# Kernel tuning notes

Measured on AMD Instinct MI355X. Metric: run time of the kernel, lower is better.

Reference implementation:

```python
import jax, jax.numpy as jnp
import numpy as np

B, N, D = 4, 1024, 1024
H, KV, HD = 16, 4, 64
S, CTX = 128, 2048
MLPD = 4096
NITER, DT = 2, 0.1


def _rms(x, w, eps=1e-6):
    return x * jax.lax.rsqrt(jnp.mean(x * x, axis=-1, keepdims=True) + eps) * w


def _gelu(x):
    return jax.nn.gelu(x, approximate=False)  # torch nn.GELU() is exact erf


def _rope(q, k, cos, sin):
    # q: [B,H,N,HD], cos/sin: [N, HD//2]; interleaved-half RoPE as in source
    q1, q2 = q[..., ::2], q[..., 1::2]
    k1, k2 = k[..., ::2], k[..., 1::2]
    c = cos[None, None]
    s = sin[None, None]
    q_rot = jnp.concatenate([q1 * c - q2 * s, q1 * s + q2 * c], axis=-1)
    k_rot = jnp.concatenate([k1 * c - k2 * s, k1 * s + k2 * c], axis=-1)
    return q_rot, k_rot


def setup_inputs():
    key = jax.random.key(0)
    ks = jax.random.split(key, 24)
    rn = lambda k, shp, s=0.02: jax.random.normal(k, shp, jnp.float32) * s
    inv = 1.0 / (10000.0 ** (jnp.arange(0, HD, 2, dtype=jnp.float32) / HD))  # [HD//2]
    ang = jnp.arange(N, dtype=jnp.float32)[:, None] * inv[None, :]
    return {
        'x': jax.random.normal(ks[0], (B, N, D), jnp.float32),
        'c': jax.random.normal(ks[1], (B, D), jnp.float32),
        'context': jax.random.normal(ks[2], (B, S, CTX), jnp.float32),
        'cos': jnp.cos(ang), 'sin': jnp.sin(ang),
        'wq': rn(ks[3], (D, D)), 'wk': rn(ks[4], (D, KV * HD)),
        'wv': rn(ks[5], (D, KV * HD)), 'wo': rn(ks[6], (D, D)),
        'cwq': rn(ks[7], (D, D)), 'cwk': rn(ks[8], (CTX, D)),
        'cwv': rn(ks[9], (CTX, D)), 'cwo': rn(ks[10], (D, D)),
        'fc1_w': rn(ks[11], (D, MLPD)), 'fc1_b': jnp.zeros((MLPD,), jnp.float32),
        'fc2_w': rn(ks[12], (MLPD, D)), 'fc2_b': jnp.zeros((D,), jnp.float32),
        'ada_w': rn(ks[13], (D, 6 * D)), 'ada_b': jnp.zeros((6 * D,), jnp.float32),
        'n1': jnp.ones((D,), jnp.float32), 'n2': jnp.ones((D,), jnp.float32), 'n3': jnp.ones((D,), jnp.float32),
        'int_w': jnp.full((D,), 0.5, jnp.float32), 'mu': jnp.zeros((D,), jnp.float32),
        'hg1_w': rn(ks[14], (D, D // 4)), 'hg1_b': jnp.zeros((D // 4,), jnp.float32),
        'hg2_w': rn(ks[15], (D // 4, 1)), 'hg2_b': jnp.zeros((1,), jnp.float32),
        'ct1_w': rn(ks[16], (2 * D, D // 2)), 'ct1_b': jnp.zeros((D // 2,), jnp.float32),
        'ct2_w': rn(ks[17], (D // 2, 3 * D)), 'ct2_b': jnp.zeros((3 * D,), jnp.float32),
        'rf1_w': rn(ks[18], (D, 2 * D)), 'rf1_b': jnp.zeros((2 * D,), jnp.float32),
        'rf2_w': rn(ks[19], (2 * D, D)), 'rf2_b': jnp.zeros((D,), jnp.float32),
    }


def _forward(x, c, context, cos, sin, wq, wk, wv, wo, cwq, cwk, cwv, cwo,
             fc1_w, fc1_b, fc2_w, fc2_b, ada_w, ada_b, n1, n2, n3, int_w, mu,
             hg1_w, hg1_b, hg2_w, hg2_b, ct1_w, ct1_b, ct2_w, ct2_b,
             rf1_w, rf1_b, rf2_w, rf2_b):
    scale = HD ** -0.5
    # AdaLN-Zero modulation from timestep conditioning c: [B, 6D]
    mod = jax.nn.silu(c) @ ada_w + ada_b
    sh_msa, sc_msa, g_msa, sh_mlp, sc_mlp, g_mlp = jnp.split(mod, 6, axis=-1)
    # --- GQA self-attention with RoPE ---
    h = _rms(x, n1) * (1.0 + sc_msa[:, None, :]) + sh_msa[:, None, :]
    q = (h @ wq).reshape(B, N, H, HD).transpose(0, 2, 1, 3)
    k = (h @ wk).reshape(B, N, KV, HD).transpose(0, 2, 1, 3)
    v = (h @ wv).reshape(B, N, KV, HD).transpose(0, 2, 1, 3)
    q, k = _rope(q, k, cos, sin)
    k = jnp.repeat(k, H // KV, axis=1)  # repeat_interleave over head dim
    v = jnp.repeat(v, H // KV, axis=1)
    attn = jax.nn.softmax(jnp.einsum('bhnd,bhmd->bhnm', q, k) * scale, axis=-1)
    sa = jnp.einsum('bhnm,bhmd->bhnd', attn, v).transpose(0, 2, 1, 3).reshape(B, N, D) @ wo
    x = x + g_msa[:, None, :] * sa
    # --- cross-attention (text conditioning) ---
    h2 = _rms(x, n2)
    qc = (h2 @ cwq).reshape(B, N, H, HD).transpose(0, 2, 1, 3)
    kc = (context @ cwk).reshape(B, S, H, HD).transpose(0, 2, 1, 3)
    vc = (context @ cwv).reshape(B, S, H, HD).transpose(0, 2, 1, 3)
    ca = jax.nn.softmax(jnp.einsum('bhnd,bhsd->bhns', qc, kc) * scale, axis=-1)
    xa = jnp.einsum('bhns,bhsd->bhnd', ca, vc).transpose(0, 2, 1, 3).reshape(B, N, D) @ cwo
    x = x + xa
    # --- AdaLN-modulated MLP ---
    h3 = _rms(x, n3) * (1.0 + sc_mlp[:, None, :]) + sh_mlp[:, None, :]
    m = _gelu(h3 @ fc1_w + fc1_b) @ fc2_w + fc2_b
    x = x + g_mlp[:, None, :] * m
    # --- IntegratorNeuron: damped-oscillator halting dynamics ---
    vst = jnp.zeros_like(x)
    integ = x
    halt_probs = []
    for _ in range(NITER):
        ctrl = _gelu(jnp.concatenate([integ, vst], axis=-1) @ ct1_w + ct1_b) @ ct2_w + ct2_b
        a_raw, b_raw, g_raw = jnp.split(ctrl, 3, axis=-1)
        alpha = jax.nn.sigmoid(a_raw)
        beta = jax.nn.softplus(b_raw)
        gate = jax.nn.sigmoid(g_raw)
        v_next = alpha * vst - beta * (integ - mu)
        x_next = integ + DT * gate * v_next
        hp = jax.nn.sigmoid(_gelu(x_next @ hg1_w + hg1_b) @ hg2_w + hg2_b)  # [B,N,1]
        refined = _gelu(x_next @ rf1_w + rf1_b) @ rf2_w + rf2_b
        integ = integ + hp * refined * int_w
        vst = v_next
        halt_probs.append(hp)
    return integ, jnp.stack(halt_probs, axis=1)


def reference(x, c, context, cos, sin, wq, wk, wv, wo, cwq, cwk, cwv, cwo,
              fc1_w, fc1_b, fc2_w, fc2_b, ada_w, ada_b, n1, n2, n3, int_w, mu,
              hg1_w, hg1_b, hg2_w, hg2_b, ct1_w, ct1_b, ct2_w, ct2_b,
              rf1_w, rf1_b, rf2_w, rf2_b):
    return _forward(x, c, context, cos, sin, wq, wk, wv, wo, cwq, cwk, cwv, cwo,
                    fc1_w, fc1_b, fc2_w, fc2_b, ada_w, ada_b, n1, n2, n3, int_w, mu,
                    hg1_w, hg1_b, hg2_w, hg2_b, ct1_w, ct1_b, ct2_w, ct2_b,
                    rf1_w, rf1_b, rf2_w, rf2_b)
```

## Files before the change

kernel.cpp:

```cpp
#include <hip/hip_runtime.h>
#include <hip/hip_bf16.h>
#include <math.h>

typedef __hip_bfloat16 bf16;
typedef unsigned short ushort;
typedef __bf16 bf16x8 __attribute__((ext_vector_type(8)));
typedef unsigned short u16x8 __attribute__((ext_vector_type(8)));
typedef float f32x4 __attribute__((ext_vector_type(4)));

#define BB 4
#define NN 1024
#define DD 1024
#define HH 16
#define KVH 4
#define HDIM 64
#define SS 128
#define CTXD 2048
#define MLPDIM 4096

__device__ __forceinline__ float bf2f(bf16 v){ return __bfloat162float(v); }
__device__ __forceinline__ bf16 f2bf(float v){ return __float2bfloat16(v); }
__device__ __forceinline__ ushort fbits(float v){ bf16 h = __float2bfloat16(v); return *(ushort*)&h; }
__device__ __forceinline__ float ubf(ushort u){ unsigned int x = ((unsigned int)u) << 16; float f; *(unsigned int*)&f = x; return f; }
__device__ __forceinline__ float sigmf_(float x){ return 1.f/(1.f+expf(-x)); }
__device__ __forceinline__ float geluf_(float x){ return 0.5f*x*(1.f+erff(x*0.70710678118f)); }

typedef const __attribute__((address_space(1))) void* gas_t;
typedef __attribute__((address_space(3))) void* las_t;
__device__ __forceinline__ void gl2lds16(const void* g, void* l){
  __builtin_amdgcn_global_load_lds((gas_t)g, (las_t)l, 16, 0, 0);
}

__global__ void k_copy4(const float4* __restrict__ in, float4* __restrict__ out, int n4){
  int i = blockIdx.x*256 + threadIdx.x;
  if (i < n4) out[i] = in[i];
}
__global__ void k_f2bfv(const float* __restrict__ in, bf16* __restrict__ out, int n){
  int i = blockIdx.x*256 + threadIdx.x;
  if (i < n) out[i] = f2bf(in[i]);
}
__global__ void k_silu(const float* __restrict__ c, float* __restrict__ out, int n){
  int i = blockIdx.x*256 + threadIdx.x;
  if (i < n){ float v = c[i]; out[i] = v*sigmf_(v); }
}
__global__ void k_zero16(unsigned short* __restrict__ p, int n){
  int i = blockIdx.x*256 + threadIdx.x;
  if (i < n) p[i] = 0;
}

__global__ __launch_bounds__(256) void k_wt(const float* __restrict__ in, bf16* __restrict__ out, int K, int N){
  __shared__ float t[64][65];
  int bn = blockIdx.x*64, bk = blockIdx.y*64;
  int tid = threadIdx.x;
  int c4 = (tid & 15)*4, r = tid >> 4;
  #pragma unroll
  for (int i = 0; i < 4; ++i){
    float4 v = *(const float4*)(in + (size_t)(bk + r + i*16)*N + bn + c4);
    t[c4+0][r+i*16] = v.x; t[c4+1][r+i*16] = v.y; t[c4+2][r+i*16] = v.z; t[c4+3][r+i*16] = v.w;
  }
  __syncthreads();
  int n = tid >> 2, k16 = (tid & 3)*16;
  bf16* orow = out + (size_t)(bn + n)*K + bk + k16;
  #pragma unroll
  for (int j = 0; j < 16; ++j) orow[j] = f2bf(t[n][k16 + j]);
}

__global__ void k_adab(const float* __restrict__ b, float* __restrict__ mod, int n){
  int idx = blockIdx.x*256 + threadIdx.x;
  if (idx < n) mod[idx] = b[idx % 6144];
}
__global__ __launch_bounds__(256) void k_ada2(const float* __restrict__ sc, const float* __restrict__ w,
                       float* __restrict__ mod){
  __shared__ float sl[4][32];
  int tid = threadIdx.x;
  int col4 = blockIdx.x*1024 + tid*4;
  int k0 = blockIdx.y*32;
  if (tid < 128) sl[tid >> 5][tid & 31] = sc[(tid >> 5)*DD + k0 + (tid & 31)];
  __syncthreads();
  f32x4 acc[4] = {};
  for (int kk = 0; kk < 32; ++kk){
    const float4 wv4 = *(const float4*)(w + (size_t)(k0 + kk)*6144 + col4);
    #pragma unroll
    for (int b = 0; b < 4; ++b){
      float s = sl[b][kk];
      acc[b][0] += s*wv4.x; acc[b][1] += s*wv4.y; acc[b][2] += s*wv4.z; acc[b][3] += s*wv4.w;
    }
  }
  #pragma unroll
  for (int b = 0; b < 4; ++b)
    #pragma unroll
    for (int j = 0; j < 4; ++j)
      atomicAdd(&mod[(size_t)b*6144 + col4 + j], acc[b][j]);
}

__global__ __launch_bounds__(256) void k_rms(const float* __restrict__ X, const float* __restrict__ w,
                      const float* __restrict__ mod, int sc_off, int sh_off,
                      bf16* __restrict__ out, int use_mod){
  __shared__ float red[256];
  int row = blockIdx.x;
  int b = row >> 10;
  int tid = threadIdx.x;
  const float* xr = X + (size_t)row*DD;
  float s = 0.f;
  #pragma unroll
  for (int i = 0; i < 4; ++i){ float v = xr[tid + i*256]; s += v*v; }
  red[tid] = s; __syncthreads();
  for (int st = 128; st > 0; st >>= 1){ if (tid < st) red[tid] += red[tid+st]; __syncthreads(); }
  float rstd = rsqrtf(red[0]*(1.f/DD) + 1e-6f);
  bf16* orow = out + (size_t)row*DD;
  const float* mrow = use_mod ? (mod + (size_t)b*6*DD) : nullptr;
  #pragma unroll
  for (int i = 0; i < 4; ++i){
    int d = tid + i*256;
    float v = xr[d]*rstd*w[d];
    if (use_mod) v = v*(1.f + mrow[sc_off + d]) + mrow[sh_off + d];
    orow[d] = f2bf(v);
  }
}

__global__ __launch_bounds__(256,2) void k_mm2(const ushort* __restrict__ A, const ushort* __restrict__ BT,
                      const float* __restrict__ bias, ushort* __restrict__ C,
                      int M, int N, int K, int act){
  __shared__ ushort As[128*64];
  __shared__ ushort Bs[128*64];
  int tid = threadIdx.x, lane = tid & 63, wv = tid >> 6;
  int l15 = lane & 15, quad = lane >> 4;
  int bm = blockIdx.y*128, bn = blockIdx.x*128;
  int wm = (wv & 1)*64, wn = (wv >> 1)*64;
  int lr = lane >> 3, lc = lane & 7;
  int ksw = (lc ^ lr) << 3;
  f32x4 acc[4][4] = {};
  const ushort* Abase = A  + (size_t)(bm + wv*32 + lr)*K + ksw;
  const ushort* Bbase = BT + (size_t)(bn + wv*32 + lr)*K + ksw;
  ushort* AsW = As + wv*2048;
  ushort* BsW = Bs + wv*2048;
  int swr = (l15 & 7) << 3;
  for (int k0 = 0; k0 < K; k0 += 64){
    #pragma unroll
    for (int i = 0; i < 4; ++i){
      gl2lds16(Abase + k0 + (size_t)(i*8)*K, AsW + i*512);
      gl2lds16(Bbase + k0 + (size_t)(i*8)*K, BsW + i*512);
    }
    __syncthreads();
    #pragma unroll
    for (int ks = 0; ks < 2; ++ks){
      bf16x8 af[4], bfr[4];
      #pragma unroll
      for (int mi = 0; mi < 4; ++mi){
        int r = wm + mi*16 + l15;
        af[mi] = __builtin_bit_cast(bf16x8, *(const uint4*)(As + r*64 + ((ks*32 + quad*8) ^ swr)));
      }
      #pragma unroll
      for (int nj = 0; nj < 4; ++nj){
        int r = wn + nj*16 + l15;
        bfr[nj] = __builtin_bit_cast(bf16x8, *(const uint4*)(Bs + r*64 + ((ks*32 + quad*8) ^ swr)));
      }
      #pragma unroll
      for (int mi = 0; mi < 4; ++mi)
        #pragma unroll
        for (int nj = 0; nj < 4; ++nj)
          acc[mi][nj] = __builtin_amdgcn_mfma_f32_16x16x32_bf16(af[mi], bfr[nj], acc[mi][nj], 0, 0, 0);
    }
    __syncthreads();
  }
  #pragma unroll
  for (int nj = 0; nj < 4; ++nj){
    int col = bn + wn + nj*16 + l15;
    float bv = bias ? bias[col] : 0.f;
    #pragma unroll
    for (int mi = 0; mi < 4; ++mi){
      #pragma unroll
      for (int r = 0; r < 4; ++r){
        int row = bm + wm + mi*16 + quad*4 + r;
        float v = acc[mi][nj][r] + bv;
        if (act) v = geluf_(v);
        C[(size_t)row*N + col] = fbits(v);
      }
    }
  }
}

__global__ __launch_bounds__(256,2) void k_mm2h(const ushort* __restrict__ A, const ushort* __restrict__ BT,
                      const float* __restrict__ bias, ushort* __restrict__ C,
                      int M, int N, int K, int act){
  __shared__ ushort As[128*64];
  __shared__ ushort Bs[64*64];
  int tid = threadIdx.x, lane = tid & 63, wv = tid >> 6;
  int l15 = lane & 15, quad = lane >> 4;
  int bm = blockIdx.y*128, bn = blockIdx.x*64;
  int wm = wv*32;
  int lr = lane >> 3, lc = lane & 7;
  int ksw = (lc ^ lr) << 3;
  f32x4 acc[2][4] = {};
  const ushort* Abase = A  + (size_t)(bm + wv*32 + lr)*K + ksw;
  const ushort* Bbase = BT + (size_t)(bn + wv*16 + lr)*K + ksw;
  ushort* AsW = As + wv*2048;
  ushort* BsW = Bs + wv*1024;
  int swr = (l15 & 7) << 3;
  for (int k0 = 0; k0 < K; k0 += 64){
    #pragma unroll
    for (int i = 0; i < 4; ++i)
      gl2lds16(Abase + k0 + (size_t)(i*8)*K, AsW + i*512);
    #pragma unroll
    for (int i = 0; i < 2; ++i)
      gl2lds16(Bbase + k0 + (size_t)(i*8)*K, BsW + i*512);
    __syncthreads();
    #pragma unroll
    for (int ks = 0; ks < 2; ++ks){
      bf16x8 af[2], bfr[4];
      #pragma unroll
      for (int mi = 0; mi < 2; ++mi){
        int r = wm + mi*16 + l15;
        af[mi] = __builtin_bit_cast(bf16x8, *(const uint4*)(As + r*64 + ((ks*32 + quad*8) ^ swr)));
      }
      #pragma unroll
      for (int nj = 0; nj < 4; ++nj){
        int r = nj*16 + l15;
        bfr[nj] = __builtin_bit_cast(bf16x8, *(const uint4*)(Bs + r*64 + ((ks*32 + quad*8) ^ swr)));
      }
      #pragma unroll
      for (int mi = 0; mi < 2; ++mi)
        #pragma unroll
        for (int nj = 0; nj < 4; ++nj)
          acc[mi][nj] = __builtin_amdgcn_mfma_f32_16x16x32_bf16(af[mi], bfr[nj], acc[mi][nj], 0, 0, 0);
    }
    __syncthreads();
  }
  #pragma unroll
  for (int nj = 0; nj < 4; ++nj){
    int col = bn + nj*16 + l15;
    float bv = bias ? bias[col] : 0.f;
    #pragma unroll
    for (int mi = 0; mi < 2; ++mi){
      #pragma unroll
      for (int r = 0; r < 4; ++r){
        int row = bm + wm + mi*16 + quad*4 + r;
        float v = acc[mi][nj][r] + bv;
        if (act) v = geluf_(v);
        C[(size_t)row*N + col] = fbits(v);
      }
    }
  }
}

__global__ void k_rope(const bf16* __restrict__ in, const float* __restrict__ cw,
                       const float* __restrict__ sw, bf16* __restrict__ out, int NHp, int n){
  int idx = blockIdx.x*256 + threadIdx.x;
  if (idx >= n) return;
  int d2 = idx & 31; int t = idx >> 5;
  int nn = t % NN; t /= NN; int h = t % NHp; int b = t / NHp;
  const bf16* base = in + ((size_t)((b*NN+nn)*NHp + h))*HDIM;
  float e = bf2f(base[2*d2]), o = bf2f(base[2*d2+1]);
  float c = cw[nn*32 + d2], s = sw[nn*32 + d2];
  bf16* ob = out + ((size_t)((b*NHp+h)*NN + nn))*HDIM;
  ob[d2]      = f2bf(e*c - o*s);
  ob[32 + d2] = f2bf(e*s + o*c);
}

__global__ void k_tr(const bf16* __restrict__ in, bf16* __restrict__ out, int T, int NHp, int n){
  int idx = blockIdx.x*256 + threadIdx.x;
  if (idx >= n) return;
  int d = idx & 63; int t = idx >> 6;
  int h = t % NHp; t /= NHp; int tok = t % T; int b = t / T;
  out[((size_t)((b*NHp+h)*T + tok))*64 + d] = in[idx];
}

__global__ void k_trv(const bf16* __restrict__ in, bf16* __restrict__ out, int T, int NHp, int n){
  int idx = blockIdx.x*256 + threadIdx.x;
  if (idx >= n) return;
  int d = idx & 63; int t = idx >> 6;
  int h = t % NHp; t /= NHp; int tok = t % T; int b = t / T;
  out[((size_t)(b*NHp+h)*64 + d)*T + tok] = in[idx];
}

__global__ __launch_bounds__(256) void k_fattn(const ushort* __restrict__ Q, const ushort* __restrict__ K,
                      const ushort* __restrict__ V, ushort* __restrict__ O,
                      int NH, int NKV, int Nq, int Nk, float scale){
  __shared__ ushort Kt[64*64];
  __shared__ ushort Vt[64*64];
  __shared__ ushort Ps[4][16*72];
  int tid = threadIdx.x, lane = tid & 63, wv = tid >> 6;
  int l15 = lane & 15, quad = lane >> 4;
  int lr = lane >> 3, lc = lane & 7;
  int ksw = (lc ^ lr) << 3;
  int swr = (l15 & 7) << 3;
  int nqt = Nq >> 6;
  int qt = blockIdx.x % nqt; int t = blockIdx.x / nqt; int h = t % NH; int b = t / NH;
  int kvh = h / (NH / NKV);
  const ushort* Kb = K + (size_t)(b*NKV+kvh)*Nk*64 + ksw;
  const ushort* Vb = V + (size_t)(b*NKV+kvh)*64*Nk + ksw;
  const ushort* Qp = Q + ((size_t)((b*NH+h)*Nq + qt*64 + wv*16 + l15))*64;
  uint4 qraw0 = *(const uint4*)(Qp + quad*8);
  uint4 qraw1 = *(const uint4*)(Qp + 32 + quad*8);
  u16x8 q0 = __builtin_bit_cast(u16x8, qraw0), q1 = __builtin_bit_cast(u16x8, qraw1);
  #pragma unroll
  for (int j = 0; j < 8; ++j){ q0[j] = fbits(ubf(q0[j])*scale); q1[j] = fbits(ubf(q1[j])*scale); }
  bf16x8 qf0 = __builtin_bit_cast(bf16x8, q0);
  bf16x8 qf1 = __builtin_bit_cast(bf16x8, q1);
  f32x4 acc[4] = {};
  float m_run[4] = {-1e30f,-1e30f,-1e30f,-1e30f};
  float l_run[4] = {0.f,0.f,0.f,0.f};
  ushort* Pw = Ps[wv];
  int wrow = wv*16;
  for (int t0 = 0; t0 < Nk; t0 += 64){
    #pragma unroll
    for (int i = 0; i < 2; ++i){
      int row = wrow + i*8 + lr;
      gl2lds16(Kb + (size_t)(t0+row)*64, Kt + (wrow + i*8)*64);
      gl2lds16(Vb + (size_t)row*Nk + t0, Vt + (wrow + i*8)*64);
    }
    __syncthreads();
    f32x4 s[4] = {};
    __builtin_amdgcn_s_setprio(1);
    #pragma unroll
    for (int nj = 0; nj < 4; ++nj){
      const ushort* kr = Kt + (nj*16+l15)*64;
      bf16x8 kf0 = __builtin_bit_cast(bf16x8, *(const uint4*)(kr + ((quad*8) ^ swr)));
      s[nj] = __builtin_amdgcn_mfma_f32_16x16x32_bf16(qf0, kf0, s[nj], 0, 0, 0);
      bf16x8 kf1 = __builtin_bit_cast(bf16x8, *(const uint4*)(kr + ((32 + quad*8) ^ swr)));
      s[nj] = __builtin_amdgcn_mfma_f32_16x16x32_bf16(qf1, kf1, s[nj], 0, 0, 0);
    }
    __builtin_amdgcn_s_setprio(0);
    float al[4];
    #pragma unroll
    for (int r = 0; r < 4; ++r){
      float tm = fmaxf(fmaxf(s[0][r], s[1][r]), fmaxf(s[2][r], s[3][r]));
      #pragma unroll
      for (int off = 8; off; off >>= 1) tm = fmaxf(tm, __shfl_xor(tm, off, 64));
      float mn = fmaxf(m_run[r], tm);
      al[r] = expf(m_run[r] - mn);
      m_run[r] = mn;
      float ts = 0.f;
      #pragma unroll
      for (int nj = 0; nj < 4; ++nj){ float p = expf(s[nj][r] - mn); s[nj][r] = p; ts += p; }
      #pragma unroll
      for (int off = 8; off; off >>= 1) ts += __shfl_xor(ts, off, 64);
      l_run[r] = l_run[r]*al[r] + ts;
    }
    #pragma unroll
    for (int nj = 0; nj < 4; ++nj){
      #pragma unroll
      for (int r = 0; r < 4; ++r){
        acc[nj][r] *= al[r];
        Pw[(quad*4+r)*72 + nj*16 + l15] = fbits(s[nj][r]);
      }
    }
    bf16x8 pf0 = __builtin_bit_cast(bf16x8, *(const uint4*)(Pw + l15*72 + quad*8));
    bf16x8 pf1 = __builtin_bit_cast(bf16x8, *(const uint4*)(Pw + l15*72 + 32 + quad*8));
    __builtin_amdgcn_s_setprio(1);
    #pragma unroll
    for (int nj = 0; nj < 4; ++nj){
      const ushort* vr = Vt + (nj*16+l15)*64;
      bf16x8 vf0 = __builtin_bit_cast(bf16x8, *(const uint4*)(vr + ((quad*8) ^ swr)));
      acc[nj] = __builtin_amdgcn_mfma_f32_16x16x32_bf16(pf0, vf0, acc[nj], 0, 0, 0);
      bf16x8 vf1 = __builtin_bit_cast(bf16x8, *(const uint4*)(vr + ((32 + quad*8) ^ swr)));
      acc[nj] = __builtin_amdgcn_mfma_f32_16x16x32_bf16(pf1, vf1, acc[nj], 0, 0, 0);
    }
    __builtin_amdgcn_s_setprio(0);
    __syncthreads();
  }
  float inv[4];
  #pragma unroll
  for (int r = 0; r < 4; ++r) inv[r] = 1.f / l_run[r];
  int nbase = qt*64 + wv*16 + quad*4;
  #pragma unroll
  for (int r = 0; r < 4; ++r){
    size_t ob = ((size_t)((b*Nq + nbase + r)*NH + h))*64;
    #pragma unroll
    for (int nj = 0; nj < 4; ++nj)
      O[ob + nj*16 + l15] = fbits(acc[nj][r]*inv[r]);
  }
}

__global__ void k_resid(float* __restrict__ X, const bf16* __restrict__ val,
                        const float* __restrict__ mod, int goff, int n){
  int i = blockIdx.x*256 + threadIdx.x;
  if (i >= n) return;
  float g = 1.f;
  if (mod){ int b = i >> 20; int d = i & 1023; g = mod[b*6144 + goff + d]; }
  X[i] += g*bf2f(val[i]);
}

__global__ void k_concat(const float* __restrict__ X, const bf16* __restrict__ V,
                         bf16* __restrict__ C, int n){
  int i = blockIdx.x*256 + threadIdx.x;
  if (i >= n) return;
  int row = i >> 11, col = i & 2047;
  C[i] = (col < 1024) ? f2bf(X[(size_t)row*1024 + col]) : V[(size_t)row*1024 + col - 1024];
}

__global__ void k_ctrl(const bf16* __restrict__ ctrl, const float* __restrict__ X,
                       bf16* __restrict__ VST, bf16* __restrict__ XN,
                       const float* __restrict__ mu, int n){
  int i = blockIdx.x*256 + threadIdx.x;
  if (i >= n) return;
  int row = i >> 10, d = i & 1023;
  const bf16* cr = ctrl + (size_t)row*3072;
  float alpha = sigmf_(bf2f(cr[d]));
  float braw  = bf2f(cr[1024 + d]);
  float beta  = fmaxf(braw, 0.f) + log1pf(expf(-fabsf(braw)));
  float gate  = sigmf_(bf2f(cr[2048 + d]));
  float vn = alpha*bf2f(VST[i]) - beta*(X[i] - mu[d]);
  VST[i] = f2bf(vn);
  XN[i]  = f2bf(X[i] + 0.1f*gate*vn);
}

__global__ __launch_bounds__(64) void k_hg2(const bf16* __restrict__ hin, const float* __restrict__ w,
                     const float* __restrict__ bb, float* __restrict__ hp,
                     float* __restrict__ oout, int it){
  int r = blockIdx.x; int lane = threadIdx.x;
  const bf16* hr = hin + (size_t)r*256;
  float s = 0.f;
  #pragma unroll
  for (int i = 0; i < 4; ++i) s += bf2f(hr[lane + i*64])*w[lane + i*64];
  for (int off = 32; off; off >>= 1) s += __shfl_xor(s, off, 64);
  if (lane == 0){
    float v = sigmf_(s + bb[0]);
    hp[r] = v;
    int b = r >> 10, nn = r & 1023;
    oout[((size_t)(b*2 + it) << 10) + nn] = v;
  }
}

__global__ void k_integ(float* __restrict__ X, const float* __restrict__ hp,
                        const bf16* __restrict__ rf, const float* __restrict__ iw, int n){
  int i = blockIdx.x*256 + threadIdx.x;
  if (i >= n) return;
  int row = i >> 10, d = i & 1023;
  X[i] += hp[row]*bf2f(rf[i])*iw[d];
}

extern "C" void kernel_launch(void* const* d_in, const int* in_sizes, int n_in,
                              void* d_out, int out_size, void* d_ws, size_t ws_size,
                              hipStream_t stream) {
  const float* x_in  = (const float*)d_in[0];
  const float* c_in  = (const float*)d_in[1];
  const float* ctx_in= (const float*)d_in[2];
  const float* cosw  = (const float*)d_in[3];
  const float* sinw  = (const float*)d_in[4];
  const float* wq    = (const float*)d_in[5];
  const float* wk    = (const float*)d_in[6];
  const float* wv    = (const float*)d_in[7];
  const float* wo    = (const float*)d_in[8];
  const float* cwq   = (const float*)d_in[9];
  const float* cwk   = (const float*)d_in[10];
  const float* cwv   = (const float*)d_in[11];
  const float* cwo   = (const float*)d_in[12];
  const float* fc1_w = (const float*)d_in[13];
  const float* fc1_b = (const float*)d_in[14];
  const float* fc2_w = (const float*)d_in[15];
  const float* fc2_b = (const float*)d_in[16];
  const float* ada_w = (const float*)d_in[17];
  const float* ada_b = (const float*)d_in[18];
  const float* n1    = (const float*)d_in[19];
  const float* n2    = (const float*)d_in[20];
  const float* n3    = (const float*)d_in[21];
  const float* int_w = (const float*)d_in[22];
  const float* mu    = (const float*)d_in[23];
  const float* hg1_w = (const float*)d_in[24];
  const float* hg1_b = (const float*)d_in[25];
  const float* hg2_w = (const float*)d_in[26];
  const float* hg2_b = (const float*)d_in[27];
  const float* ct1_w = (const float*)d_in[28];
  const float* ct1_b = (const float*)d_in[29];
  const float* ct2_w = (const float*)d_in[30];
  const float* ct2_b = (const float*)d_in[31];
  const float* rf1_w = (const float*)d_in[32];
  const float* rf1_b = (const float*)d_in[33];
  const float* rf2_w = (const float*)d_in[34];
  const float* rf2_b = (const float*)d_in[35];

  float* out_f  = (float*)d_out;
  float* out_hp = out_f + (size_t)BB*NN*DD;

  char* wsb = (char*)d_ws;
  const size_t Mi = 1u << 20;
  float* X  = (float*)wsb;
  bf16*  Hh = (bf16*)(wsb + 16*Mi);
  bf16*  Qb = (bf16*)(wsb + 24*Mi);
  bf16*  R  = (bf16*)(wsb + 32*Mi);
  bf16*  QR  = R;
  bf16*  SAb = R + 4*Mi;
  bf16*  KP  = R + 8*Mi;
  bf16*  VP  = R + 9*Mi;
  bf16*  KR  = R + 10*Mi;
  bf16*  VR  = R + 11*Mi;
  bf16*  CTXB= R + 12*Mi;
  bf16*  BIG = R;
  bf16*  CT1 = R + 12*Mi;
  bf16*  HG1 = R + 12*Mi;
  bf16*  RFO = R + 8*Mi;
  float* SIL = (float*)(wsb + 64*Mi);
  float* MOD = SIL + 4096;
  float* HP  = MOD + 24576;
  bf16*  VST = Qb;
  bf16*  XN  = Hh;
  bf16* WT   = (bf16*)(wsb + 65*Mi);
  bf16* wqT  = WT;
  bf16* wkT  = wqT  + 1048576;
  bf16* wvT  = wkT  + 262144;
  bf16* woT  = wvT  + 262144;
  bf16* cwqT = woT  + 1048576;
  bf16* cwkT = cwqT + 1048576;
  bf16* cwvT = cwkT + 2097152;
  bf16* cwoT = cwvT + 2097152;
  bf16* fc1T = cwoT + 1048576;
  bf16* fc2T = fc1T + 4194304;
  bf16* ct1T = fc2T + 4194304;
  bf16* ct2T = ct1T + 1048576;
  bf16* rf1T = ct2T + 1572864;
  bf16* rf2T = rf1T + 2097152;
  bf16* hg1T = rf2T + 2097152;

  const int NT = BB*NN*DD;
  const float scale = 0.125f;
  #define G1(n) dim3(((n)+255)/256), dim3(256)
  #define WTR(src,dst,K,N) k_wt<<<dim3((N)/64,(K)/64), dim3(256), 0, stream>>>((src),(dst),(K),(N))
  #define MM(Aptr,BTptr,biasptr,Cptr,M,N,K,act) \
    k_mm2<<<dim3((N)/128,(M)/128), dim3(256), 0, stream>>>((const ushort*)(Aptr),(const ushort*)(BTptr),(biasptr),(ushort*)(Cptr),(M),(N),(K),(act))
  #define MMH(Aptr,BTptr,biasptr,Cptr,M,N,K,act) \
    k_mm2h<<<dim3((N)/64,(M)/128), dim3(256), 0, stream>>>((const ushort*)(Aptr),(const ushort*)(BTptr),(biasptr),(ushort*)(Cptr),(M),(N),(K),(act))

  WTR(wq,   wqT, 1024, 1024);
  WTR(wk,   wkT, 1024, 256);
  WTR(wv,   wvT, 1024, 256);
  WTR(wo,   woT, 1024, 1024);
  WTR(cwq,  cwqT,1024, 1024);
  WTR(cwk,  cwkT,2048, 1024);
  WTR(cwv,  cwvT,2048, 1024);
  WTR(cwo,  cwoT,1024, 1024);
  WTR(fc1_w,fc1T,1024, 4096);
  WTR(fc2_w,fc2T,4096, 1024);
  WTR(ct1_w,ct1T,2048, 512);
  WTR(ct2_w,ct2T,512,  3072);
  WTR(rf1_w,rf1T,1024, 2048);
  WTR(rf2_w,rf2T,2048, 1024);
  WTR(hg1_w,hg1T,1024, 256);

  k_copy4<<<G1(NT/4), 0, stream>>>((const float4*)x_in, (float4*)X, NT/4);
  k_silu<<<G1(BB*DD), 0, stream>>>(c_in, SIL, BB*DD);
  k_adab<<<G1(BB*6144), 0, stream>>>(ada_b, MOD, BB*6144);
  k_ada2<<<dim3(6,32), dim3(256), 0, stream>>>(SIL, ada_w, MOD);

  k_rms<<<dim3(4096), dim3(256), 0, stream>>>(X, n1, MOD, DD, 0, Hh, 1);
  MM(Hh, wqT, nullptr, Qb, 4096, 1024, 1024, 0);
  MMH(Hh, wkT, nullptr, KP, 4096, 256, 1024, 0);
  MMH(Hh, wvT, nullptr, VP, 4096, 256, 1024, 0);
  k_rope<<<G1(BB*HH*NN*32), 0, stream>>>(Qb, cosw, sinw, QR, HH, BB*HH*NN*32);
  k_rope<<<G1(BB*KVH*NN*32), 0, stream>>>(KP, cosw, sinw, KR, KVH, BB*KVH*NN*32);
  k_trv<<<G1(BB*NN*KVH*64), 0, stream>>>(VP, VR, NN, KVH, BB*NN*KVH*64);
  k_fattn<<<dim3(BB*HH*(NN/64)), dim3(256), 0, stream>>>((const ushort*)QR, (const ushort*)KR,
      (const ushort*)VR, (ushort*)SAb, HH, KVH, NN, NN, scale);
  MM(SAb, woT, nullptr, Hh, 4096, 1024, 1024, 0);
  k_resid<<<G1(NT), 0, stream>>>(X, Hh, MOD, 2*DD, NT);

  k_rms<<<dim3(4096), dim3(256), 0, stream>>>(X, n2, nullptr, 0, 0, Hh, 0);
  MM(Hh, cwqT, nullptr, Qb, 4096, 1024, 1024, 0);
  k_tr<<<G1(NT), 0, stream>>>(Qb, QR, NN, HH, NT);
  k_f2bfv<<<G1(BB*SS*CTXD), 0, stream>>>(ctx_in, CTXB, BB*SS*CTXD);
  MMH(CTXB, cwkT, nullptr, KP, 512, 1024, 2048, 0);
  MMH(CTXB, cwvT, nullptr, VP, 512, 1024, 2048, 0);
  k_tr<<<G1(BB*SS*HH*64), 0, stream>>>(KP, KR, SS, HH, BB*SS*HH*64);
  k_trv<<<G1(BB*SS*HH*64), 0, stream>>>(VP, VR, SS, HH, BB*SS*HH*64);
  k_fattn<<<dim3(BB*HH*(NN/64)), dim3(256), 0, stream>>>((const ushort*)QR, (const ushort*)KR,
      (const ushort*)VR, (ushort*)SAb, HH, HH, NN, SS, scale);
  MM(SAb, cwoT, nullptr, Hh, 4096, 1024, 1024, 0);
  k_resid<<<G1(NT), 0, stream>>>(X, Hh, nullptr, 0, NT);

  k_rms<<<dim3(4096), dim3(256), 0, stream>>>(X, n3, MOD, 4*DD, 3*DD, Hh, 1);
  MM(Hh, fc1T, fc1_b, BIG, 4096, 4096, 1024, 1);
  MM(BIG, fc2T, fc2_b, Qb, 4096, 1024, 4096, 0);
  k_resid<<<G1(NT), 0, stream>>>(X, Qb, MOD, 5*DD, NT);

  k_zero16<<<G1(NT), 0, stream>>>((unsigned short*)VST, NT);
  for (int it = 0; it < 2; ++it){
    k_concat<<<G1(2*NT), 0, stream>>>(X, VST, BIG, 2*NT);
    MMH(BIG, ct1T, ct1_b, CT1, 4096, 512, 2048, 1);
    MM(CT1, ct2T, ct2_b, BIG, 4096, 3072, 512, 0);
    k_ctrl<<<G1(NT), 0, stream>>>(BIG, X, VST, XN, mu, NT);
    MMH(XN, hg1T, hg1_b, HG1, 4096, 256, 1024, 1);
    k_hg2<<<dim3(4096), dim3(64), 0, stream>>>(HG1, hg2_w, hg2_b, HP, out_hp, it);
    MM(XN, rf1T, rf1_b, BIG, 4096, 2048, 1024, 1);
    MM(BIG, rf2T, rf2_b, RFO, 4096, 1024, 2048, 0);
    k_integ<<<G1(NT), 0, stream>>>(X, HP, RFO, int_w, NT);
  }
  k_copy4<<<G1(NT/4), 0, stream>>>((const float4*)X, (float4*)out_f, NT/4);
  #undef G1
  #undef WTR
  #undef MM
  #undef MMH
}
```

Baseline: 1.125 ms.

## Use exp2 softmax with lazy max rescale in flash attention; drop input copy

The flash-attention kernel folds log2(e) into the Q scale and uses exp2f. It keeps per-lane partial row sums, reducing them across lanes once at the end instead of every tile. The running max and accumulator are rescaled only when some row's max grows by more than a threshold, which skips the shuffle-max and rescale work on most tiles at the cost of larger unnormalised exponents. Separately, the initial copy of x into X is removed: the first RMSNorm reads the input directly and the first residual kernel writes base plus update.

```diff
diff --git a/kernel.cpp b/kernel.cpp
--- a/kernel.cpp
+++ b/kernel.cpp
@@ -290,16 +290,17 @@
   const ushort* Kb = K + (size_t)(b*NKV+kvh)*Nk*64 + ksw;
   const ushort* Vb = V + (size_t)(b*NKV+kvh)*64*Nk + ksw;
   const ushort* Qp = Q + ((size_t)((b*NH+h)*Nq + qt*64 + wv*16 + l15))*64;
+  float qscale = scale * 1.44269504f;
   uint4 qraw0 = *(const uint4*)(Qp + quad*8);
   uint4 qraw1 = *(const uint4*)(Qp + 32 + quad*8);
   u16x8 q0 = __builtin_bit_cast(u16x8, qraw0), q1 = __builtin_bit_cast(u16x8, qraw1);
   #pragma unroll
-  for (int j = 0; j < 8; ++j){ q0[j] = fbits(ubf(q0[j])*scale); q1[j] = fbits(ubf(q1[j])*scale); }
+  for (int j = 0; j < 8; ++j){ q0[j] = fbits(ubf(q0[j])*qscale); q1[j] = fbits(ubf(q1[j])*qscale); }
   bf16x8 qf0 = __builtin_bit_cast(bf16x8, q0);
   bf16x8 qf1 = __builtin_bit_cast(bf16x8, q1);
   f32x4 acc[4] = {};
-  float m_run[4] = {-1e30f,-1e30f,-1e30f,-1e30f};
-  float l_run[4] = {0.f,0.f,0.f,0.f};
+  float m_run[4]  = {0.f,0.f,0.f,0.f};
+  float l_part[4] = {0.f,0.f,0.f,0.f};
   ushort* Pw = Ps[wv];
   int wrow = wv*16;
   for (int t0 = 0; t0 < Nk; t0 += 64){
@@ -321,30 +322,37 @@
       s[nj] = __builtin_amdgcn_mfma_f32_16x16x32_bf16(qf1, kf1, s[nj], 0, 0, 0);
     }
     __builtin_amdgcn_s_setprio(0);
-    float al[4];
-    #pragma unroll
-    for (int r = 0; r < 4; ++r){
-      float tm = fmaxf(fmaxf(s[0][r], s[1][r]), fmaxf(s[2][r], s[3][r]));
-      #pragma unroll
-      for (int off = 8; off; off >>= 1) tm = fmaxf(tm, __shfl_xor(tm, off, 64));
-      float mn = fmaxf(m_run[r], tm);
-      al[r] = expf(m_run[r] - mn);
-      m_run[r] = mn;
-      float ts = 0.f;
-      #pragma unroll
-      for (int nj = 0; nj < 4; ++nj){ float p = expf(s[nj][r] - mn); s[nj][r] = p; ts += p; }
-      #pragma unroll
-      for (int off = 8; off; off >>= 1) ts += __shfl_xor(ts, off, 64);
-      l_run[r] = l_run[r]*al[r] + ts;
-    }
-    #pragma unroll
-    for (int nj = 0; nj < 4; ++nj){
+    float tl[4];
+    #pragma unroll
+    for (int r = 0; r < 4; ++r)
+      tl[r] = fmaxf(fmaxf(s[0][r], s[1][r]), fmaxf(s[2][r], s[3][r]));
+    float dmax = fmaxf(fmaxf(tl[0]-m_run[0], tl[1]-m_run[1]),
+                       fmaxf(tl[2]-m_run[2], tl[3]-m_run[3]));
+    if (__any(dmax > 8.f)){
       #pragma unroll
       for (int r = 0; r < 4; ++r){
-        acc[nj][r] *= al[r];
-        Pw[(quad*4+r)*72 + nj*16 + l15] = fbits(s[nj][r]);
-      }
-    }
+        float tm = tl[r];
+        #pragma unroll
+        for (int off = 8; off; off >>= 1) tm = fmaxf(tm, __shfl_xor(tm, off, 64));
+        float mn = fmaxf(m_run[r], tm);
+        float al = exp2f(m_run[r] - mn);
+        m_run[r] = mn;
+        l_part[r] *= al;
+        #pragma unroll
+        for (int nj = 0; nj < 4; ++nj) acc[nj][r] *= al;
+      }
+    }
+    #pragma unroll
+    for (int nj = 0; nj < 4; ++nj)
+      #pragma unroll
+      for (int r = 0; r < 4; ++r){
+        float p = exp2f(s[nj][r] - m_run[r]);
+        s[nj][r] = p;
+        Pw[(quad*4+r)*72 + nj*16 + l15] = fbits(p);
+      }
+    #pragma unroll
+    for (int r = 0; r < 4; ++r)
+      l_part[r] += (s[0][r]+s[1][r]) + (s[2][r]+s[3][r]);
     bf16x8 pf0 = __builtin_bit_cast(bf16x8, *(const uint4*)(Pw + l15*72 + quad*8));
     bf16x8 pf1 = __builtin_bit_cast(bf16x8, *(const uint4*)(Pw + l15*72 + 32 + quad*8));
     __builtin_amdgcn_s_setprio(1);
@@ -361,7 +369,12 @@
   }
   float inv[4];
   #pragma unroll
-  for (int r = 0; r < 4; ++r) inv[r] = 1.f / l_run[r];
+  for (int r = 0; r < 4; ++r){
+    float ls = l_part[r];
+    #pragma unroll
+    for (int off = 8; off; off >>= 1) ls += __shfl_xor(ls, off, 64);
+    inv[r] = 1.f / ls;
+  }
   int nbase = qt*64 + wv*16 + quad*4;
   #pragma unroll
   for (int r = 0; r < 4; ++r){
@@ -372,13 +385,15 @@
   }
 }
 
-__global__ void k_resid(float* __restrict__ X, const bf16* __restrict__ val,
+__global__ void k_resid(float* __restrict__ X, const float* __restrict__ base,
+                        const bf16* __restrict__ val,
                         const float* __restrict__ mod, int goff, int n){
   int i = blockIdx.x*256 + threadIdx.x;
   if (i >= n) return;
   float g = 1.f;
   if (mod){ int b = i >> 20; int d = i & 1023; g = mod[b*6144 + goff + d]; }
-  X[i] += g*bf2f(val[i]);
+  float x0 = base ? base[i] : X[i];
+  X[i] = x0 + g*bf2f(val[i]);
 }
 
 __global__ void k_concat(const float* __restrict__ X, const bf16* __restrict__ V,
@@ -537,12 +552,11 @@
   WTR(rf2_w,rf2T,2048, 1024);
   WTR(hg1_w,hg1T,1024, 256);
 
-  k_copy4<<<G1(NT/4), 0, stream>>>((const float4*)x_in, (float4*)X, NT/4);
   k_silu<<<G1(BB*DD), 0, stream>>>(c_in, SIL, BB*DD);
   k_adab<<<G1(BB*6144), 0, stream>>>(ada_b, MOD, BB*6144);
   k_ada2<<<dim3(6,32), dim3(256), 0, stream>>>(SIL, ada_w, MOD);
 
-  k_rms<<<dim3(4096), dim3(256), 0, stream>>>(X, n1, MOD, DD, 0, Hh, 1);
+  k_rms<<<dim3(4096), dim3(256), 0, stream>>>(x_in, n1, MOD, DD, 0, Hh, 1);
   MM(Hh, wqT, nullptr, Qb, 4096, 1024, 1024, 0);
   MMH(Hh, wkT, nullptr, KP, 4096, 256, 1024, 0);
   MMH(Hh, wvT, nullptr, VP, 4096, 256, 1024, 0);
@@ -552,7 +566,7 @@
   k_fattn<<<dim3(BB*HH*(NN/64)), dim3(256), 0, stream>>>((const ushort*)QR, (const ushort*)KR,
       (const ushort*)VR, (ushort*)SAb, HH, KVH, NN, NN, scale);
   MM(SAb, woT, nullptr, Hh, 4096, 1024, 1024, 0);
-  k_resid<<<G1(NT), 0, stream>>>(X, Hh, MOD, 2*DD, NT);
+  k_resid<<<G1(NT), 0, stream>>>(X, x_in, Hh, MOD, 2*DD, NT);
 
   k_rms<<<dim3(4096), dim3(256), 0, stream>>>(X, n2, nullptr, 0, 0, Hh, 0);
   MM(Hh, cwqT, nullptr, Qb, 4096, 1024, 1024, 0);
@@ -565,12 +579,12 @@
   k_fattn<<<dim3(BB*HH*(NN/64)), dim3(256), 0, stream>>>((const ushort*)QR, (const ushort*)KR,
       (const ushort*)VR, (ushort*)SAb, HH, HH, NN, SS, scale);
   MM(SAb, cwoT, nullptr, Hh, 4096, 1024, 1024, 0);
-  k_resid<<<G1(NT), 0, stream>>>(X, Hh, nullptr, 0, NT);
+  k_resid<<<G1(NT), 0, stream>>>(X, nullptr, Hh, nullptr, 0, NT);
 
   k_rms<<<dim3(4096), dim3(256), 0, stream>>>(X, n3, MOD, 4*DD, 3*DD, Hh, 1);
   MM(Hh, fc1T, fc1_b, BIG, 4096, 4096, 1024, 1);
   MM(BIG, fc2T, fc2_b, Qb, 4096, 1024, 4096, 0);
-  k_resid<<<G1(NT), 0, stream>>>(X, Qb, MOD, 5*DD, NT);
+  k_resid<<<G1(NT), 0, stream>>>(X, nullptr, Qb, MOD, 5*DD, NT);
 
   k_zero16<<<G1(NT), 0, stream>>>((unsigned short*)VST, NT);
   for (int it = 0; it < 2; ++it){
```

Measured after the change: 1.086 ms. -3.4%, faster.
